# Performance work log

Hardware: AMD Instinct MI355X
Metric: run time of the kernel (lower is better)

The kernel has to match this reference:

```python
import jax, jax.numpy as jnp
import numpy as np

T, B, E, H = 2048, 2, 1024, 16
D = E // H
NEG = -1e18


def setup_inputs() -> dict:
    key = jax.random.key(0)
    k1, k2, k3, k4, k5 = jax.random.split(key, 5)
    return {
        "query": jax.random.normal(k1, (T, B, E), dtype=jnp.float32),
        "in_proj_weight": jax.random.normal(k2, (3 * E, E), dtype=jnp.float32) * 0.02,
        "in_proj_bias": jax.random.normal(k3, (3 * E,), dtype=jnp.float32) * 0.02,
        "out_proj_weight": jax.random.normal(k4, (E, E), dtype=jnp.float32) * 0.02,
        "out_proj_bias": jax.random.normal(k5, (E,), dtype=jnp.float32) * 0.02,
    }


def reference(query, in_proj_weight, in_proj_bias, out_proj_weight, out_proj_bias):
    # Self-attention (qkv_same), mask_future_timesteps=True, no padding mask,
    # eval mode (dropout p=0), need_weights=True.
    tgt_len, bsz, embed_dim = query.shape
    # fused in-projection: [T,B,3E]
    qkv = jnp.einsum("tbe,fe->tbf", query, in_proj_weight) + in_proj_bias
    q, k, v = jnp.split(qkv, 3, axis=-1)
    q = q * (D ** -0.5)
    # [T,B,E] -> [B*H, T, D]
    def to_heads(x):
        return x.reshape(tgt_len, bsz * H, D).transpose(1, 0, 2)
    q, k, v = to_heads(q), to_heads(k), to_heads(v)
    # scores: [B*H, T, T]
    scores = jnp.einsum("ntd,nsd->nts", q, k)
    causal = jnp.triu(jnp.full((tgt_len, tgt_len), NEG, dtype=scores.dtype), k=1)
    scores = scores + causal[None, :, :]
    attn_weights = jax.nn.softmax(scores, axis=-1)
    # context: [B*H, T, D] -> [T, B, E]
    ctx = jnp.einsum("nts,nsd->ntd", attn_weights, v)
    ctx = ctx.transpose(1, 0, 2).reshape(tgt_len, bsz, embed_dim)
    out = jnp.einsum("tbe,fe->tbf", ctx, out_proj_weight) + out_proj_bias
    # averaged attention weights over heads: [B, T, T]
    avg_w = attn_weights.reshape(bsz, H, tgt_len, tgt_len).sum(axis=1) / H
    return (out, avg_w)
```

## Files before the change

kernel.cpp:

```cpp
#include <hip/hip_runtime.h>
#include <math.h>

#define T_LEN 2048
#define BSZ 2
#define EMB 1024
#define NHEAD 16
#define HDIM 64
#define QK_LD 2048

typedef __attribute__((ext_vector_type(8))) short short8v;
typedef __attribute__((ext_vector_type(4))) float floatx4;

__device__ __forceinline__ short f2bf(float f) {
    unsigned u = __float_as_uint(f);
    u += 0x7fffu + ((u >> 16) & 1u);
    return (short)(u >> 16);
}

__device__ __forceinline__ void async16(const short* g, short* l) {
    __builtin_amdgcn_global_load_lds(
        (const __attribute__((address_space(1))) void*)g,
        (__attribute__((address_space(3))) void*)l, 16, 0, 0);
}

__global__ __launch_bounds__(256) void f32_to_bf16_k(const float* __restrict__ src,
                                                     short* __restrict__ dst, int n) {
    int i = (blockIdx.x * 256 + threadIdx.x) * 4;
    if (i >= n) return;
    float4 v = *(const float4*)(src + i);
    short4 o = make_short4(f2bf(v.x), f2bf(v.y), f2bf(v.z), f2bf(v.w));
    *(short4*)(dst + i) = o;
}

__global__ __launch_bounds__(256) void gemm_bf16(const short* __restrict__ A,
        const short* __restrict__ B, const float* __restrict__ bias,
        void* __restrict__ Cout, short* __restrict__ vTout,
        int M, int N, int K, int scale_cols, int out_bf16, int ldC) {
    __shared__ short As[128][32];
    __shared__ short Bs[128][32];
    const int tid = threadIdx.x;
    const int m0 = blockIdx.x * 128, n0 = blockIdx.y * 128;
    const int lane = tid & 63, w = tid >> 6;
    const int q = lane >> 4, r = lane & 15;
    const int wr = w >> 1, wc = w & 1;

    const int srow = lane >> 2;
    const int spos = lane & 3;
    const int rowL = w * 16 + srow;
    const int rowH = 64 + rowL;
    const int csrc = spos ^ ((rowL >> 1) & 3);
    const short* gA0 = A + (size_t)(m0 + rowL) * K + csrc * 8;
    const short* gA1 = A + (size_t)(m0 + rowH) * K + csrc * 8;
    const short* gB0 = B + (size_t)(n0 + rowL) * K + csrc * 8;
    const short* gB1 = B + (size_t)(n0 + rowH) * K + csrc * 8;
    short* lA0 = &As[w * 16][0];
    short* lA1 = &As[64 + w * 16][0];
    short* lB0 = &Bs[w * 16][0];
    short* lB1 = &Bs[64 + w * 16][0];

    floatx4 acc[4][4];
    #pragma unroll
    for (int a = 0; a < 4; ++a)
        #pragma unroll
        for (int b2 = 0; b2 < 4; ++b2)
            #pragma unroll
            for (int e = 0; e < 4; ++e) acc[a][b2][e] = 0.f;

    for (int k0 = 0; k0 < K; k0 += 32) {
        __syncthreads();
        async16(gA0 + k0, lA0);
        async16(gA1 + k0, lA1);
        async16(gB0 + k0, lB0);
        async16(gB1 + k0, lB1);
        __syncthreads();
        short8v af[4], bfr[4];
        #pragma unroll
        for (int mb = 0; mb < 4; ++mb) {
            int row = wr * 64 + mb * 16 + r;
            af[mb] = *(const short8v*)&As[row][(q ^ ((row >> 1) & 3)) * 8];
        }
        #pragma unroll
        for (int nb = 0; nb < 4; ++nb) {
            int row = wc * 64 + nb * 16 + r;
            bfr[nb] = *(const short8v*)&Bs[row][(q ^ ((row >> 1) & 3)) * 8];
        }
        #pragma unroll
        for (int mb = 0; mb < 4; ++mb)
            #pragma unroll
            for (int nb = 0; nb < 4; ++nb)
                acc[mb][nb] = __builtin_amdgcn_mfma_f32_16x16x32_bf16(af[mb], bfr[nb], acc[mb][nb], 0, 0, 0);
    }

    #pragma unroll
    for (int nb = 0; nb < 4; ++nb) {
        const int col = n0 + wc * 64 + nb * 16 + r;
        const float bi = bias[col];
        const float sc = (col < scale_cols) ? 0.125f : 1.0f;
        if (vTout && col >= 2 * EMB) {
            const int e = col - 2 * EMB;
            #pragma unroll
            for (int mb = 0; mb < 4; ++mb) {
                const int base = m0 + wr * 64 + mb * 16 + q * 4;
                float v0 = acc[mb][nb][0] + bi, v1 = acc[mb][nb][1] + bi;
                float v2 = acc[mb][nb][2] + bi, v3 = acc[mb][nb][3] + bi;
                unsigned lo = (unsigned short)f2bf(v0) | ((unsigned)(unsigned short)f2bf(v2) << 16);
                unsigned hi = (unsigned short)f2bf(v1) | ((unsigned)(unsigned short)f2bf(v3) << 16);
                *(unsigned*)&vTout[(size_t)e * T_LEN + (base >> 1)]         = lo;
                *(unsigned*)&vTout[((size_t)EMB + e) * T_LEN + (base >> 1)] = hi;
            }
        } else {
            #pragma unroll
            for (int mb = 0; mb < 4; ++mb)
                #pragma unroll
                for (int i = 0; i < 4; ++i) {
                    const int rowg = m0 + wr * 64 + mb * 16 + q * 4 + i;
                    const float v = (acc[mb][nb][i] + bi) * sc;
                    if (out_bf16) ((short*)Cout)[(size_t)rowg * ldC + col] = f2bf(v);
                    else          ((float*)Cout)[(size_t)rowg * ldC + col] = v;
                }
        }
    }
}

__global__ __launch_bounds__(256) void flash_fwd(const short* __restrict__ qk,
        const short* __restrict__ vT, short* __restrict__ ctx,
        float* __restrict__ Lr) {
    __shared__ short Ks[128][64];
    __shared__ short Vt[64][128];
    __shared__ short Ps[2][64][64];
    __shared__ float Lred[4][64];
    const int tid = threadIdx.x;
    const int bh = blockIdx.x;
    const int pairi = blockIdx.y;
    const int b = bh >> 4, h = bh & 15;
    const int lane = tid & 63, w = tid >> 6;
    const int q = lane >> 4, r = lane & 15;
    const int RS = BSZ * QK_LD;

    const short* qbase = qk + (size_t)b * QK_LD + h * HDIM;
    const short* kbase = qbase + EMB;
    const short* vbase = vT + ((size_t)b * EMB + h * HDIM) * T_LEN;

    for (int pass = 0; pass < 2; ++pass) {
        const int tt = pass ? (31 - pairi) : pairi;
        const int t0 = tt << 6;
        __syncthreads();
        {
            const int sr = tid >> 3, c8 = tid & 7;
            *(int4*)&Ps[0][sr][(c8 ^ (sr & 7)) * 8] =
                *(const int4*)(qbase + (size_t)(t0 + sr) * RS + c8 * 8);
            *(int4*)&Ps[0][sr + 32][(c8 ^ ((sr + 32) & 7)) * 8] =
                *(const int4*)(qbase + (size_t)(t0 + sr + 32) * RS + c8 * 8);
        }
        __syncthreads();
        short8v qf[4][2];
        #pragma unroll
        for (int mb = 0; mb < 4; ++mb)
            #pragma unroll
            for (int ks = 0; ks < 2; ++ks) {
                int row = mb * 16 + r;
                qf[mb][ks] = *(const short8v*)&Ps[0][row][((ks * 4 + q) ^ (row & 7)) * 8];
            }

        float l_part[4][4];
        floatx4 o[4];
        #pragma unroll
        for (int mb = 0; mb < 4; ++mb)
            #pragma unroll
            for (int i = 0; i < 4; ++i) l_part[mb][i] = 0.f;
        #pragma unroll
        for (int nb = 0; nb < 4; ++nb)
            #pragma unroll
            for (int e = 0; e < 4; ++e) o[nb][e] = 0.f;

        const int ntiles = tt + 1;
        int s2 = 0;
        for (; s2 + 2 <= ntiles; s2 += 2) {
            __syncthreads();
            {
                const int sr = tid >> 1, cb = (tid & 1) * 4;
                const short* kp = kbase + (size_t)(s2 * 64 + sr) * RS;
                #pragma unroll
                for (int u = 0; u < 4; ++u) {
                    const int c = cb + u;
                    *(int4*)&Ks[sr][(c ^ (sr & 7)) * 8] = *(const int4*)(kp + c * 8);
                }
                const int vr = tid >> 2, vb0 = (tid & 3) * 4;
                const short* vp = vbase + (size_t)vr * T_LEN + s2 * 64;
                #pragma unroll
                for (int u = 0; u < 4; ++u) {
                    const int c = vb0 + u;
                    const int pc = (c & 8) | ((c & 7) ^ (vr & 7));
                    *(int4*)&Vt[vr][pc * 8] = *(const int4*)(vp + c * 8);
                }
            }
            __syncthreads();
            #pragma unroll
            for (int t2 = 0; t2 < 2; ++t2) {
                floatx4 sf[4];
                #pragma unroll
                for (int mb = 0; mb < 4; ++mb)
                    #pragma unroll
                    for (int e = 0; e < 4; ++e) sf[mb][e] = 0.f;
                #pragma unroll
                for (int ks = 0; ks < 2; ++ks) {
                    const int krow = t2 * 64 + w * 16 + r;
                    short8v kf = *(const short8v*)&Ks[krow][((ks * 4 + q) ^ (krow & 7)) * 8];
                    #pragma unroll
                    for (int mb = 0; mb < 4; ++mb)
                        sf[mb] = __builtin_amdgcn_mfma_f32_16x16x32_bf16(qf[mb][ks], kf, sf[mb], 0, 0, 0);
                }
                const bool diag = (s2 + t2 == tt);
                #pragma unroll
                for (int mb = 0; mb < 4; ++mb)
                    #pragma unroll
                    for (int i = 0; i < 4; ++i) {
                        const int rl = mb * 16 + q * 4 + i;
                        float p = (diag && (w * 16 + r > rl)) ? 0.f : __expf(sf[mb][i]);
                        l_part[mb][i] += p;
                        const int c = (w * 2 + (r >> 3)) ^ (rl & 7);
                        Ps[t2][rl][c * 8 + (r & 7)] = f2bf(p);
                    }
            }
            __syncthreads();
            #pragma unroll
            for (int ks = 0; ks < 2; ++ks) {
                const int prow = w * 16 + r;
                const int pcp = ((ks * 4 + q) ^ (prow & 7)) * 8;
                short8v pfA = *(const short8v*)&Ps[0][prow][pcp];
                short8v pfB = *(const short8v*)&Ps[1][prow][pcp];
                #pragma unroll
                for (int nb = 0; nb < 4; ++nb) {
                    const int vrow = nb * 16 + r;
                    const int pcv = (ks * 4 + q) ^ (vrow & 7);
                    short8v vfA = *(const short8v*)&Vt[vrow][pcv * 8];
                    short8v vfB = *(const short8v*)&Vt[vrow][(8 | pcv) * 8];
                    o[nb] = __builtin_amdgcn_mfma_f32_16x16x32_bf16(pfA, vfA, o[nb], 0, 0, 0);
                    o[nb] = __builtin_amdgcn_mfma_f32_16x16x32_bf16(pfB, vfB, o[nb], 0, 0, 0);
                }
            }
        }
        if (s2 < ntiles) {
            __syncthreads();
            {
                const int sr = tid >> 2, cb = (tid & 3) * 2;
                const short* kp = kbase + (size_t)(s2 * 64 + sr) * RS;
                const short* vp = vbase + (size_t)sr * T_LEN + s2 * 64;
                #pragma unroll
                for (int u = 0; u < 2; ++u) {
                    const int c = cb + u;
                    *(int4*)&Ks[sr][(c ^ (sr & 7)) * 8] = *(const int4*)(kp + c * 8);
                    *(int4*)&Vt[sr][(c ^ (sr & 7)) * 8] = *(const int4*)(vp + c * 8);
                }
            }
            __syncthreads();
            floatx4 sf[4];
            #pragma unroll
            for (int mb = 0; mb < 4; ++mb)
                #pragma unroll
                for (int e = 0; e < 4; ++e) sf[mb][e] = 0.f;
            #pragma unroll
            for (int ks = 0; ks < 2; ++ks) {
                const int krow = w * 16 + r;
                short8v kf = *(const short8v*)&Ks[krow][((ks * 4 + q) ^ (krow & 7)) * 8];
                #pragma unroll
                for (int mb = 0; mb < 4; ++mb)
                    sf[mb] = __builtin_amdgcn_mfma_f32_16x16x32_bf16(qf[mb][ks], kf, sf[mb], 0, 0, 0);
            }
            #pragma unroll
            for (int mb = 0; mb < 4; ++mb)
                #pragma unroll
                for (int i = 0; i < 4; ++i) {
                    const int rl = mb * 16 + q * 4 + i;
                    float p = (w * 16 + r > rl) ? 0.f : __expf(sf[mb][i]);
                    l_part[mb][i] += p;
                    const int c = (w * 2 + (r >> 3)) ^ (rl & 7);
                    Ps[0][rl][c * 8 + (r & 7)] = f2bf(p);
                }
            __syncthreads();
            #pragma unroll
            for (int ks = 0; ks < 2; ++ks) {
                const int prow = w * 16 + r;
                short8v pf = *(const short8v*)&Ps[0][prow][((ks * 4 + q) ^ (prow & 7)) * 8];
                #pragma unroll
                for (int nb = 0; nb < 4; ++nb) {
                    const int vrow = nb * 16 + r;
                    short8v vf = *(const short8v*)&Vt[vrow][(((ks * 4 + q) ^ (vrow & 7))) * 8];
                    o[nb] = __builtin_amdgcn_mfma_f32_16x16x32_bf16(pf, vf, o[nb], 0, 0, 0);
                }
            }
        }

        #pragma unroll
        for (int mb = 0; mb < 4; ++mb)
            #pragma unroll
            for (int i = 0; i < 4; ++i) {
                float v = l_part[mb][i];
                v += __shfl_xor(v, 1, 16);
                v += __shfl_xor(v, 2, 16);
                v += __shfl_xor(v, 4, 16);
                v += __shfl_xor(v, 8, 16);
                if (r == 0) Lred[w][mb * 16 + q * 4 + i] = v;
            }
        __syncthreads();
        if (tid < 64) {
            float s = Lred[0][tid] + Lred[1][tid] + Lred[2][tid] + Lred[3][tid];
            Lr[(size_t)bh * T_LEN + t0 + tid] = s;
            Lred[0][tid] = s;
        }
        __syncthreads();
        #pragma unroll
        for (int i = 0; i < 4; ++i) {
            const int tl = w * 16 + q * 4 + i;
            const float inv = 1.0f / Lred[0][tl];
            #pragma unroll
            for (int nb = 0; nb < 4; ++nb)
                ctx[((size_t)(t0 + tl) * BSZ + b) * EMB + h * HDIM + nb * 16 + r] =
                    f2bf(o[nb][i] * inv);
        }
    }
}

__global__ __launch_bounds__(256) void avg_w_k(const short* __restrict__ qk,
        const float* __restrict__ Lr, float* __restrict__ avg) {
    const int s0 = blockIdx.x * 64, t0 = blockIdx.y * 64, b = blockIdx.z;
    const int tid = threadIdx.x;
    float* outb = avg + (size_t)b * T_LEN * T_LEN;
    if (s0 > t0) {
        const int ty = tid >> 4, tx = tid & 15;
        const float4 z = make_float4(0.f, 0.f, 0.f, 0.f);
        #pragma unroll
        for (int i = 0; i < 4; ++i)
            *(float4*)&outb[(size_t)(t0 + ty * 4 + i) * T_LEN + s0 + tx * 4] = z;
        return;
    }
    __shared__ short Qs[64][128];
    __shared__ short Ks[64][128];
    __shared__ float Lbuf[NHEAD][64];
    const int lane = tid & 63, w = tid >> 6;
    const int q = lane >> 4, r = lane & 15;
    const int srow = tid >> 2, c4 = (tid & 3) * 4;
    const short* qbase = qk + (size_t)b * QK_LD;
    const int RS = BSZ * QK_LD;

    #pragma unroll
    for (int u = 0; u < 4; ++u) {
        const int li = tid * 4 + u;
        const int h = li >> 6, tl = li & 63;
        Lbuf[h][tl] = 0.0625f / Lr[(size_t)(b * NHEAD + h) * T_LEN + t0 + tl];
    }

    floatx4 acc[4];
    #pragma unroll
    for (int nb = 0; nb < 4; ++nb)
        #pragma unroll
        for (int e = 0; e < 4; ++e) acc[nb][e] = 0.f;

    for (int hp = 0; hp < 8; ++hp) {
        const short* qh = qbase + hp * 128;
        const short* kh = qbase + EMB + hp * 128;
        __syncthreads();
        #pragma unroll
        for (int u = 0; u < 4; ++u) {
            const int c = c4 + u;
            const int pc = (c & 8) | ((c & 7) ^ (srow & 7));
            *(int4*)&Qs[srow][pc * 8] =
                *(const int4*)(qh + (size_t)(t0 + srow) * RS + c * 8);
            *(int4*)&Ks[srow][pc * 8] =
                *(const int4*)(kh + (size_t)(s0 + srow) * RS + c * 8);
        }
        __syncthreads();

        #pragma unroll
        for (int hs = 0; hs < 2; ++hs) {
            const int h = hp * 2 + hs;
            floatx4 sf[4];
            #pragma unroll
            for (int nb = 0; nb < 4; ++nb)
                #pragma unroll
                for (int e = 0; e < 4; ++e) sf[nb][e] = 0.f;
            #pragma unroll
            for (int ks = 0; ks < 2; ++ks) {
                const int qrow = w * 16 + r;
                short8v qfr = *(const short8v*)
                    &Qs[qrow][((hs * 8) | ((ks * 4 + q) ^ (qrow & 7))) * 8];
                #pragma unroll
                for (int nb = 0; nb < 4; ++nb) {
                    const int krow = nb * 16 + r;
                    short8v kfr = *(const short8v*)
                        &Ks[krow][((hs * 8) | ((ks * 4 + q) ^ (krow & 7))) * 8];
                    sf[nb] = __builtin_amdgcn_mfma_f32_16x16x32_bf16(qfr, kfr, sf[nb], 0, 0, 0);
                }
            }
            #pragma unroll
            for (int i = 0; i < 4; ++i) {
                const int tl = w * 16 + q * 4 + i;
                const float inv = Lbuf[h][tl];
                #pragma unroll
                for (int nb = 0; nb < 4; ++nb) {
                    float e = (s0 == t0 && (nb * 16 + r > tl))
                              ? 0.f : __expf(sf[nb][i]) * inv;
                    acc[nb][i] += e;
                }
            }
        }
    }

    #pragma unroll
    for (int i = 0; i < 4; ++i) {
        const int t = t0 + w * 16 + q * 4 + i;
        #pragma unroll
        for (int nb = 0; nb < 4; ++nb)
            outb[(size_t)t * T_LEN + s0 + nb * 16 + r] = acc[nb][i];
    }
}

extern "C" void kernel_launch(void* const* d_in, const int* in_sizes, int n_in,
                              void* d_out, int out_size, void* d_ws, size_t ws_size,
                              hipStream_t stream) {
    (void)in_sizes; (void)n_in; (void)out_size; (void)ws_size;
    const float* query = (const float*)d_in[0];
    const float* w_in  = (const float*)d_in[1];
    const float* b_in  = (const float*)d_in[2];
    const float* w_out = (const float*)d_in[3];
    const float* b_out = (const float*)d_in[4];

    float* out = (float*)d_out;
    float* avg = out + (size_t)T_LEN * BSZ * EMB;

    short* ws     = (short*)d_ws;
    short* wb_in  = ws;
    short* wb_out = wb_in  + (size_t)3072 * 1024;
    short* qkb    = wb_out + (size_t)1024 * 1024;
    short* vTb    = qkb    + (size_t)4096 * 2048;
    short* ctxb   = vTb    + (size_t)BSZ * EMB * T_LEN;
    float* Lr     = (float*)(ctxb + (size_t)4096 * 1024);
    short* qb     = ctxb;

    f32_to_bf16_k<<<4096, 256, 0, stream>>>(query, qb,     4096 * 1024);
    f32_to_bf16_k<<<3072, 256, 0, stream>>>(w_in,  wb_in,  3072 * 1024);
    f32_to_bf16_k<<<1024, 256, 0, stream>>>(w_out, wb_out, 1024 * 1024);

    gemm_bf16<<<dim3(32, 24), 256, 0, stream>>>(qb, wb_in, b_in, qkb, vTb,
                                                4096, 3072, 1024, EMB, 1, QK_LD);
    flash_fwd<<<dim3(32, 16), 256, 0, stream>>>(qkb, vTb, ctxb, Lr);
    avg_w_k<<<dim3(32, 32, 2), 256, 0, stream>>>(qkb, Lr, avg);
    gemm_bf16<<<dim3(32, 8), 256, 0, stream>>>(ctxb, wb_out, b_out, out, (short*)0,
                                               4096, 1024, 1024, 0, 0, 1024);
}
```

Before: 250.8 us.

## Split flash_fwd paired query tiles into separate blocks and load K/V asynchronously to LDS

The flash attention kernel previously had each block process two query tiles (i and 31-i) in sequence. Now each block handles one tile, the grid doubles to 32x32, and blockIdx.y is reversed so the heaviest tiles launch first. The main K/V tile loads switch from register-staged global loads to global_load_lds async copies, with per-lane swizzled source addresses precomputed outside the loop. This trades the explicit pairwise load balancing for more blocks and less register and VGPR traffic during loads. It relies on the swizzled async layout matching what the LDS readers expect.

```diff
diff --git a/kernel.cpp b/kernel.cpp
--- a/kernel.cpp
+++ b/kernel.cpp
@@ -131,7 +131,8 @@
     __shared__ float Lred[4][64];
     const int tid = threadIdx.x;
     const int bh = blockIdx.x;
-    const int pairi = blockIdx.y;
+    const int tt = 31 - blockIdx.y;
+    const int t0 = tt << 6;
     const int b = bh >> 4, h = bh & 15;
     const int lane = tid & 63, w = tid >> 6;
     const int q = lane >> 4, r = lane & 15;
@@ -141,183 +142,181 @@
     const short* kbase = qbase + EMB;
     const short* vbase = vT + ((size_t)b * EMB + h * HDIM) * T_LEN;
 
-    for (int pass = 0; pass < 2; ++pass) {
-        const int tt = pass ? (31 - pairi) : pairi;
-        const int t0 = tt << 6;
+    const int krow0 = w * 32 + (lane >> 3);
+    const short* kg = kbase + (size_t)krow0 * RS + ((lane & 7) ^ (krow0 & 7)) * 8;
+    const int vrow0 = w * 16 + (lane >> 4);
+    const short* vg[4];
+    #pragma unroll
+    for (int j = 0; j < 4; ++j) {
+        const int vr = vrow0 + j * 4;
+        const int gc = ((lane & 15) & 8) | (((lane & 15) & 7) ^ (vr & 7));
+        vg[j] = vbase + (size_t)vr * T_LEN + gc * 8;
+    }
+
+    {
+        const int sr = tid >> 3, c8 = tid & 7;
+        *(int4*)&Ps[0][sr][(c8 ^ (sr & 7)) * 8] =
+            *(const int4*)(qbase + (size_t)(t0 + sr) * RS + c8 * 8);
+        *(int4*)&Ps[0][sr + 32][(c8 ^ ((sr + 32) & 7)) * 8] =
+            *(const int4*)(qbase + (size_t)(t0 + sr + 32) * RS + c8 * 8);
+    }
+    __syncthreads();
+    short8v qf[4][2];
+    #pragma unroll
+    for (int mb = 0; mb < 4; ++mb)
+        #pragma unroll
+        for (int ks = 0; ks < 2; ++ks) {
+            int row = mb * 16 + r;
+            qf[mb][ks] = *(const short8v*)&Ps[0][row][((ks * 4 + q) ^ (row & 7)) * 8];
+        }
+
+    float l_part[4][4];
+    floatx4 o[4];
+    #pragma unroll
+    for (int mb = 0; mb < 4; ++mb)
+        #pragma unroll
+        for (int i = 0; i < 4; ++i) l_part[mb][i] = 0.f;
+    #pragma unroll
+    for (int nb = 0; nb < 4; ++nb)
+        #pragma unroll
+        for (int e = 0; e < 4; ++e) o[nb][e] = 0.f;
+
+    const int ntiles = tt + 1;
+    int s2 = 0;
+    for (; s2 + 2 <= ntiles; s2 += 2) {
         __syncthreads();
         {
-            const int sr = tid >> 3, c8 = tid & 7;
-            *(int4*)&Ps[0][sr][(c8 ^ (sr & 7)) * 8] =
-                *(const int4*)(qbase + (size_t)(t0 + sr) * RS + c8 * 8);
-            *(int4*)&Ps[0][sr + 32][(c8 ^ ((sr + 32) & 7)) * 8] =
-                *(const int4*)(qbase + (size_t)(t0 + sr + 32) * RS + c8 * 8);
-        }
-        __syncthreads();
-        short8v qf[4][2];
-        #pragma unroll
-        for (int mb = 0; mb < 4; ++mb)
+            const short* kgr = kg + (size_t)(s2 * 64) * RS;
+            #pragma unroll
+            for (int j = 0; j < 4; ++j)
+                async16(kgr + (size_t)(j * 8) * RS, &Ks[w * 32 + j * 8][0]);
+            #pragma unroll
+            for (int j = 0; j < 4; ++j)
+                async16(vg[j] + s2 * 64, &Vt[w * 16 + j * 4][0]);
+        }
+        __syncthreads();
+        #pragma unroll
+        for (int t2 = 0; t2 < 2; ++t2) {
+            floatx4 sf[4];
+            #pragma unroll
+            for (int mb = 0; mb < 4; ++mb)
+                #pragma unroll
+                for (int e = 0; e < 4; ++e) sf[mb][e] = 0.f;
             #pragma unroll
             for (int ks = 0; ks < 2; ++ks) {
-                int row = mb * 16 + r;
-                qf[mb][ks] = *(const short8v*)&Ps[0][row][((ks * 4 + q) ^ (row & 7)) * 8];
-            }
-
-        float l_part[4][4];
-        floatx4 o[4];
-        #pragma unroll
-        for (int mb = 0; mb < 4; ++mb)
-            #pragma unroll
-            for (int i = 0; i < 4; ++i) l_part[mb][i] = 0.f;
-        #pragma unroll
-        for (int nb = 0; nb < 4; ++nb)
-            #pragma unroll
-            for (int e = 0; e < 4; ++e) o[nb][e] = 0.f;
-
-        const int ntiles = tt + 1;
-        int s2 = 0;
-        for (; s2 + 2 <= ntiles; s2 += 2) {
-            __syncthreads();
-            {
-                const int sr = tid >> 1, cb = (tid & 1) * 4;
-                const short* kp = kbase + (size_t)(s2 * 64 + sr) * RS;
-                #pragma unroll
-                for (int u = 0; u < 4; ++u) {
-                    const int c = cb + u;
-                    *(int4*)&Ks[sr][(c ^ (sr & 7)) * 8] = *(const int4*)(kp + c * 8);
-                }
-                const int vr = tid >> 2, vb0 = (tid & 3) * 4;
-                const short* vp = vbase + (size_t)vr * T_LEN + s2 * 64;
-                #pragma unroll
-                for (int u = 0; u < 4; ++u) {
-                    const int c = vb0 + u;
-                    const int pc = (c & 8) | ((c & 7) ^ (vr & 7));
-                    *(int4*)&Vt[vr][pc * 8] = *(const int4*)(vp + c * 8);
-                }
-            }
-            __syncthreads();
-            #pragma unroll
-            for (int t2 = 0; t2 < 2; ++t2) {
-                floatx4 sf[4];
-                #pragma unroll
-                for (int mb = 0; mb < 4; ++mb)
-                    #pragma unroll
-                    for (int e = 0; e < 4; ++e) sf[mb][e] = 0.f;
-                #pragma unroll
-                for (int ks = 0; ks < 2; ++ks) {
-                    const int krow = t2 * 64 + w * 16 + r;
-                    short8v kf = *(const short8v*)&Ks[krow][((ks * 4 + q) ^ (krow & 7)) * 8];
-                    #pragma unroll
-                    for (int mb = 0; mb < 4; ++mb)
-                        sf[mb] = __builtin_amdgcn_mfma_f32_16x16x32_bf16(qf[mb][ks], kf, sf[mb], 0, 0, 0);
-                }
-                const bool diag = (s2 + t2 == tt);
-                #pragma unroll
-                for (int mb = 0; mb < 4; ++mb)
-                    #pragma unroll
-                    for (int i = 0; i < 4; ++i) {
-                        const int rl = mb * 16 + q * 4 + i;
-                        float p = (diag && (w * 16 + r > rl)) ? 0.f : __expf(sf[mb][i]);
-                        l_part[mb][i] += p;
-                        const int c = (w * 2 + (r >> 3)) ^ (rl & 7);
-                        Ps[t2][rl][c * 8 + (r & 7)] = f2bf(p);
-                    }
-            }
-            __syncthreads();
-            #pragma unroll
-            for (int ks = 0; ks < 2; ++ks) {
-                const int prow = w * 16 + r;
-                const int pcp = ((ks * 4 + q) ^ (prow & 7)) * 8;
-                short8v pfA = *(const short8v*)&Ps[0][prow][pcp];
-                short8v pfB = *(const short8v*)&Ps[1][prow][pcp];
-                #pragma unroll
-                for (int nb = 0; nb < 4; ++nb) {
-                    const int vrow = nb * 16 + r;
-                    const int pcv = (ks * 4 + q) ^ (vrow & 7);
-                    short8v vfA = *(const short8v*)&Vt[vrow][pcv * 8];
-                    short8v vfB = *(const short8v*)&Vt[vrow][(8 | pcv) * 8];
-                    o[nb] = __builtin_amdgcn_mfma_f32_16x16x32_bf16(pfA, vfA, o[nb], 0, 0, 0);
-                    o[nb] = __builtin_amdgcn_mfma_f32_16x16x32_bf16(pfB, vfB, o[nb], 0, 0, 0);
-                }
-            }
-        }
-        if (s2 < ntiles) {
-            __syncthreads();
-            {
-                const int sr = tid >> 2, cb = (tid & 3) * 2;
-                const short* kp = kbase + (size_t)(s2 * 64 + sr) * RS;
-                const short* vp = vbase + (size_t)sr * T_LEN + s2 * 64;
-                #pragma unroll
-                for (int u = 0; u < 2; ++u) {
-                    const int c = cb + u;
-                    *(int4*)&Ks[sr][(c ^ (sr & 7)) * 8] = *(const int4*)(kp + c * 8);
-                    *(int4*)&Vt[sr][(c ^ (sr & 7)) * 8] = *(const int4*)(vp + c * 8);
-                }
-            }
-            __syncthreads();
-            floatx4 sf[4];
-            #pragma unroll
-            for (int mb = 0; mb < 4; ++mb)
-                #pragma unroll
-                for (int e = 0; e < 4; ++e) sf[mb][e] = 0.f;
-            #pragma unroll
-            for (int ks = 0; ks < 2; ++ks) {
-                const int krow = w * 16 + r;
+                const int krow = t2 * 64 + w * 16 + r;
                 short8v kf = *(const short8v*)&Ks[krow][((ks * 4 + q) ^ (krow & 7)) * 8];
                 #pragma unroll
                 for (int mb = 0; mb < 4; ++mb)
                     sf[mb] = __builtin_amdgcn_mfma_f32_16x16x32_bf16(qf[mb][ks], kf, sf[mb], 0, 0, 0);
             }
+            const bool diag = (s2 + t2 == tt);
             #pragma unroll
             for (int mb = 0; mb < 4; ++mb)
                 #pragma unroll
                 for (int i = 0; i < 4; ++i) {
                     const int rl = mb * 16 + q * 4 + i;
-                    float p = (w * 16 + r > rl) ? 0.f : __expf(sf[mb][i]);
+                    float p = (diag && (w * 16 + r > rl)) ? 0.f : __expf(sf[mb][i]);
                     l_part[mb][i] += p;
                     const int c = (w * 2 + (r >> 3)) ^ (rl & 7);
-                    Ps[0][rl][c * 8 + (r & 7)] = f2bf(p);
+                    Ps[t2][rl][c * 8 + (r & 7)] = f2bf(p);
                 }
-            __syncthreads();
-            #pragma unroll
-            for (int ks = 0; ks < 2; ++ks) {
-                const int prow = w * 16 + r;
-                short8v pf = *(const short8v*)&Ps[0][prow][((ks * 4 + q) ^ (prow & 7)) * 8];
-                #pragma unroll
-                for (int nb = 0; nb < 4; ++nb) {
-                    const int vrow = nb * 16 + r;
-                    short8v vf = *(const short8v*)&Vt[vrow][(((ks * 4 + q) ^ (vrow & 7))) * 8];
-                    o[nb] = __builtin_amdgcn_mfma_f32_16x16x32_bf16(pf, vf, o[nb], 0, 0, 0);
-                }
-            }
-        }
-
+        }
+        __syncthreads();
+        #pragma unroll
+        for (int ks = 0; ks < 2; ++ks) {
+            const int prow = w * 16 + r;
+            const int pcp = ((ks * 4 + q) ^ (prow & 7)) * 8;
+            short8v pfA = *(const short8v*)&Ps[0][prow][pcp];
+            short8v pfB = *(const short8v*)&Ps[1][prow][pcp];
+            #pragma unroll
+            for (int nb = 0; nb < 4; ++nb) {
+                const int vrow = nb * 16 + r;
+                const int pcv = (ks * 4 + q) ^ (vrow & 7);
+                short8v vfA = *(const short8v*)&Vt[vrow][pcv * 8];
+                short8v vfB = *(const short8v*)&Vt[vrow][(8 | pcv) * 8];
+                o[nb] = __builtin_amdgcn_mfma_f32_16x16x32_bf16(pfA, vfA, o[nb], 0, 0, 0);
+                o[nb] = __builtin_amdgcn_mfma_f32_16x16x32_bf16(pfB, vfB, o[nb], 0, 0, 0);
+            }
+        }
+    }
+    if (s2 < ntiles) {
+        __syncthreads();
+        {
+            const int sr = tid >> 2, cb = (tid & 3) * 2;
+            const short* kp = kbase + (size_t)(s2 * 64 + sr) * RS;
+            const short* vp = vbase + (size_t)sr * T_LEN + s2 * 64;
+            #pragma unroll
+            for (int u = 0; u < 2; ++u) {
+                const int c = cb + u;
+                *(int4*)&Ks[sr][(c ^ (sr & 7)) * 8] = *(const int4*)(kp + c * 8);
+                *(int4*)&Vt[sr][(c ^ (sr & 7)) * 8] = *(const int4*)(vp + c * 8);
+            }
+        }
+        __syncthreads();
+        floatx4 sf[4];
         #pragma unroll
         for (int mb = 0; mb < 4; ++mb)
             #pragma unroll
+            for (int e = 0; e < 4; ++e) sf[mb][e] = 0.f;
+        #pragma unroll
+        for (int ks = 0; ks < 2; ++ks) {
+            const int krow = w * 16 + r;
+            short8v kf = *(const short8v*)&Ks[krow][((ks * 4 + q) ^ (krow & 7)) * 8];
+            #pragma unroll
+            for (int mb = 0; mb < 4; ++mb)
+                sf[mb] = __builtin_amdgcn_mfma_f32_16x16x32_bf16(qf[mb][ks], kf, sf[mb], 0, 0, 0);
+        }
+        #pragma unroll
+        for (int mb = 0; mb < 4; ++mb)
+            #pragma unroll
             for (int i = 0; i < 4; ++i) {
-                float v = l_part[mb][i];
-                v += __shfl_xor(v, 1, 16);
-                v += __shfl_xor(v, 2, 16);
-                v += __shfl_xor(v, 4, 16);
-                v += __shfl_xor(v, 8, 16);
-                if (r == 0) Lred[w][mb * 16 + q * 4 + i] = v;
-            }
-        __syncthreads();
-        if (tid < 64) {
-            float s = Lred[0][tid] + Lred[1][tid] + Lred[2][tid] + Lred[3][tid];
-            Lr[(size_t)bh * T_LEN + t0 + tid] = s;
-            Lred[0][tid] = s;
-        }
-        __syncthreads();
+                const int rl = mb * 16 + q * 4 + i;
+                float p = (w * 16 + r > rl) ? 0.f : __expf(sf[mb][i]);
+                l_part[mb][i] += p;
+                const int c = (w * 2 + (r >> 3)) ^ (rl & 7);
+                Ps[0][rl][c * 8 + (r & 7)] = f2bf(p);
+            }
+        __syncthreads();
+        #pragma unroll
+        for (int ks = 0; ks < 2; ++ks) {
+            const int prow = w * 16 + r;
+            short8v pf = *(const short8v*)&Ps[0][prow][((ks * 4 + q) ^ (prow & 7)) * 8];
+            #pragma unroll
+            for (int nb = 0; nb < 4; ++nb) {
+                const int vrow = nb * 16 + r;
+                short8v vf = *(const short8v*)&Vt[vrow][(((ks * 4 + q) ^ (vrow & 7))) * 8];
+                o[nb] = __builtin_amdgcn_mfma_f32_16x16x32_bf16(pf, vf, o[nb], 0, 0, 0);
+            }
+        }
+    }
+
+    #pragma unroll
+    for (int mb = 0; mb < 4; ++mb)
         #pragma unroll
         for (int i = 0; i < 4; ++i) {
-            const int tl = w * 16 + q * 4 + i;
-            const float inv = 1.0f / Lred[0][tl];
-            #pragma unroll
-            for (int nb = 0; nb < 4; ++nb)
-                ctx[((size_t)(t0 + tl) * BSZ + b) * EMB + h * HDIM + nb * 16 + r] =
-                    f2bf(o[nb][i] * inv);
-        }
+            float v = l_part[mb][i];
+            v += __shfl_xor(v, 1, 16);
+            v += __shfl_xor(v, 2, 16);
+            v += __shfl_xor(v, 4, 16);
+            v += __shfl_xor(v, 8, 16);
+            if (r == 0) Lred[w][mb * 16 + q * 4 + i] = v;
+        }
+    __syncthreads();
+    if (tid < 64) {
+        float s = Lred[0][tid] + Lred[1][tid] + Lred[2][tid] + Lred[3][tid];
+        Lr[(size_t)bh * T_LEN + t0 + tid] = s;
+        Lred[0][tid] = s;
+    }
+    __syncthreads();
+    #pragma unroll
+    for (int i = 0; i < 4; ++i) {
+        const int tl = w * 16 + q * 4 + i;
+        const float inv = 1.0f / Lred[0][tl];
+        #pragma unroll
+        for (int nb = 0; nb < 4; ++nb)
+            ctx[((size_t)(t0 + tl) * BSZ + b) * EMB + h * HDIM + nb * 16 + r] =
+                f2bf(o[nb][i] * inv);
     }
 }
 
@@ -443,7 +442,7 @@
 
     gemm_bf16<<<dim3(32, 24), 256, 0, stream>>>(qb, wb_in, b_in, qkb, vTb,
                                                 4096, 3072, 1024, EMB, 1, QK_LD);
-    flash_fwd<<<dim3(32, 16), 256, 0, stream>>>(qkb, vTb, ctxb, Lr);
+    flash_fwd<<<dim3(32, 32), 256, 0, stream>>>(qkb, vTb, ctxb, Lr);
     avg_w_k<<<dim3(32, 32, 2), 256, 0, stream>>>(qkb, Lr, avg);
     gemm_bf16<<<dim3(32, 8), 256, 0, stream>>>(ctxb, wb_out, b_out, out, (short*)0,
                                                4096, 1024, 1024, 0, 0, 1024);
```

After: 244.1 us. 1.03x faster.
